# Kernel optimization log

Hardware: AMD Instinct MI355X
Metric: run time of the kernel (lower is better)

## Reference

```python
import jax, jax.numpy as jnp
import numpy as np

N = 100000   # nodes
E = 600000   # edges
D = 128      # in_dim == out_dim
ED = 6       # edge_dim
LN_EPS = 1e-5


def setup_inputs() -> dict:
    key = jax.random.key(0)
    ks = jax.random.split(key, 12)
    s = 1.0 / np.sqrt(D)
    se = 1.0 / np.sqrt(ED)
    return {
        "x": jax.random.normal(ks[0], (N, D), dtype=jnp.float32),
        "edge_index": jax.random.randint(ks[1], (2, E), 0, N, dtype=jnp.int64),
        "edge_attr": jax.random.normal(ks[2], (E, ED), dtype=jnp.float32),
        "batch": jnp.zeros((N,), dtype=jnp.int64),
        "W_e": jax.random.uniform(ks[3], (ED, D), jnp.float32, -se, se),
        "b_e": jax.random.uniform(ks[4], (D,), jnp.float32, -se, se),
        "eps": jnp.zeros((), dtype=jnp.float32),  # GINE train_eps init 0
        "W1": jax.random.uniform(ks[5], (D, D), jnp.float32, -s, s),
        "b1": jax.random.uniform(ks[6], (D,), jnp.float32, -s, s),
        "W2": jax.random.uniform(ks[7], (D, D), jnp.float32, -s, s),
        "b2": jax.random.uniform(ks[8], (D,), jnp.float32, -s, s),
        "gamma": jnp.ones((D,), dtype=jnp.float32),
        "beta": jnp.zeros((D,), dtype=jnp.float32),
    }


def reference(x, edge_index, edge_attr, batch, W_e, b_e, eps, W1, b1, W2, b2, gamma, beta):
    src, dst = edge_index[0], edge_index[1]
    # edge embedding: Linear(edge_dim -> in_dim)
    edge_emb = edge_attr @ W_e + b_e                      # [E, D]
    # GINEConv message: ReLU(x_j + edge_emb), scatter-add to target nodes
    msg = jax.nn.relu(x[src] + edge_emb)                  # [E, D]
    agg = jax.ops.segment_sum(msg, dst, num_segments=N)   # [N, D]
    h = (1.0 + eps) * x + agg                             # [N, D]
    # GINE nn: Linear -> ReLU -> Linear
    h = jax.nn.relu(h @ W1 + b1) @ W2 + b2                # [N, D]
    # LayerNorm over feature dim
    mu = jnp.mean(h, axis=-1, keepdims=True)
    var = jnp.var(h, axis=-1, keepdims=True)
    h = (h - mu) * jax.lax.rsqrt(var + LN_EPS) * gamma + beta
    # activation=True -> ReLU; dropout identity in eval mode
    return jax.nn.relu(h)
```

## Files before the change

### kernel.cpp

```cpp
#include <hip/hip_runtime.h>
#include <stdint.h>

#define NN 100000
#define EE 600000
#define DD 128

typedef _Float16 half8 __attribute__((ext_vector_type(8)));
typedef _Float16 h2 __attribute__((ext_vector_type(2)));
typedef float f32x4 __attribute__((ext_vector_type(4)));

static __device__ __forceinline__ uint32_t pack2(float a, float b) {
    h2 h; h.x = (_Float16)a; h.y = (_Float16)b;
    return __builtin_bit_cast(uint32_t, h);
}
static __device__ __forceinline__ h2 cvt22(float2 f) {
    h2 r; r.x = (_Float16)f.x; r.y = (_Float16)f.y; return r;
}
static __device__ __forceinline__ h2 bc_lo(h2 v) { h2 r; r.x = v.x; r.y = v.x; return r; }
static __device__ __forceinline__ h2 bc_hi(h2 v) { h2 r; r.x = v.y; r.y = v.y; return r; }

static __device__ __forceinline__ uint32_t edge_msg2(uint32_t rY, uint32_t rZ, uint32_t rW,
                                                     uint32_t xv, uint32_t bb,
                                                     uint32_t w0, uint32_t w1, uint32_t w2,
                                                     uint32_t w3, uint32_t w4, uint32_t w5)
{
    uint32_t m;
    asm("v_pk_fma_f16 %0, %1, %2, %3 op_sel:[0,0,0] op_sel_hi:[0,1,1]"
        : "=v"(m) : "v"(rY), "v"(w0), "v"(bb));
    asm("v_pk_fma_f16 %0, %1, %2, %0 op_sel:[1,0,0] op_sel_hi:[1,1,1]" : "+v"(m) : "v"(rY), "v"(w1));
    asm("v_pk_fma_f16 %0, %1, %2, %0 op_sel:[0,0,0] op_sel_hi:[0,1,1]" : "+v"(m) : "v"(rZ), "v"(w2));
    asm("v_pk_fma_f16 %0, %1, %2, %0 op_sel:[1,0,0] op_sel_hi:[1,1,1]" : "+v"(m) : "v"(rZ), "v"(w3));
    asm("v_pk_fma_f16 %0, %1, %2, %0 op_sel:[0,0,0] op_sel_hi:[0,1,1]" : "+v"(m) : "v"(rW), "v"(w4));
    asm("v_pk_fma_f16 %0, %1, %2, %0 op_sel:[1,0,0] op_sel_hi:[1,1,1]" : "+v"(m) : "v"(rW), "v"(w5));
    asm("v_pk_add_f16 %0, %0, %1" : "+v"(m) : "v"(xv));
    asm("v_pk_max_f16 %0, %0, 0" : "+v"(m));
    return m;
}

#define NB_HIST ((EE + 255) / 256)
#define NB_CONV (NN * DD / 4 / 256)
template<bool CONV>
__global__ __launch_bounds__(256)
void setup_kernel(const int* __restrict__ ei, const float* __restrict__ x,
                  const float* __restrict__ W1, const float* __restrict__ W2,
                  int* __restrict__ counts, uint32_t* __restrict__ xh,
                  _Float16* __restrict__ w1h, _Float16* __restrict__ w2h)
{
    const int nbc = CONV ? NB_CONV : 0;
    const int b = blockIdx.x, tid = threadIdx.x;
    if (b < NB_HIST) {
        int e = b * 256 + tid;
        if (e < EE) atomicAdd(&counts[ei[EE + e]], 1);
    } else if (CONV && b < NB_HIST + nbc) {
        int i = (b - NB_HIST) * 256 + tid;
        float4 v = ((const float4*)x)[i];
        uint2 o; o.x = pack2(v.x, v.y); o.y = pack2(v.z, v.w);
        ((uint2*)xh)[i] = o;
    } else {
        int t = (b - NB_HIST - nbc) * 256 + tid;
        if (t < 2 * DD * DD) {
            int which = t >> 14;
            int idx = t & (DD * DD - 1);
            int k = idx >> 7, d = idx & 127;
            float wv = (which ? W2 : W1)[k * DD + d];
            int kt = k >> 5, kr = k & 31;
            int grp = kr >> 3, j = kr & 7;
            int nt = d >> 4, cc = d & 15;
            int off = ((kt * 8 + nt) * 64 + grp * 16 + cc) * 8 + j;
            (which ? w2h : w1h)[off] = (_Float16)wv;
        }
    }
}

__global__ __launch_bounds__(256)
void scan_blocks(const int* __restrict__ counts, int* __restrict__ startv,
                 int* __restrict__ bsum)
{
    const int t = threadIdx.x;
    const int idx = blockIdx.x * 1024 + t * 4;
    int4 v = {0, 0, 0, 0};
    if (idx < NN) v = *(const int4*)(counts + idx);
    int s1 = v.x + v.y, s2 = s1 + v.z, s3 = s2 + v.w;
    const int lane = t & 63;
    int q = s3;
#pragma unroll
    for (int off = 1; off < 64; off <<= 1) {
        int u = __shfl_up(q, off, 64);
        if (lane >= off) q += u;
    }
    __shared__ int wsum[4];
    if (lane == 63) wsum[t >> 6] = q;
    __syncthreads();
    const int w = t >> 6;
    int pre = 0;
    if (w > 0) pre += wsum[0];
    if (w > 1) pre += wsum[1];
    if (w > 2) pre += wsum[2];
    const int excl = (q - s3) + pre;
    if (idx < NN) {
        int4 o = {excl, excl + v.x, excl + s1, excl + s2};
        *(int4*)(startv + idx) = o;
    }
    __syncthreads();
    if (t == 0) bsum[blockIdx.x] = wsum[0] + wsum[1] + wsum[2] + wsum[3];
}

__global__ __launch_bounds__(128)
void scan_top(const int* __restrict__ bsum, int* __restrict__ boff)
{
    __shared__ int sm[128];
    const int t = threadIdx.x;
    const int NB = (NN + 1023) / 1024;
    int v = (t < NB) ? bsum[t] : 0;
    sm[t] = v;
    __syncthreads();
#pragma unroll
    for (int off = 1; off < 128; off <<= 1) {
        int u = (t >= off) ? sm[t - off] : 0;
        __syncthreads();
        sm[t] += u;
        __syncthreads();
    }
    boff[t] = sm[t] - v;
}

__global__ __launch_bounds__(256)
void scatter_rec(const int* __restrict__ ei, const float* __restrict__ ea,
                 const int* __restrict__ start, const int* __restrict__ boff,
                 int* __restrict__ cursor, float* __restrict__ rec)
{
    int e = blockIdx.x * 256 + threadIdx.x;
    if (e >= EE) return;
    int dst = ei[EE + e];
    int src = ei[e];
    int pos = start[dst] + boff[dst >> 10] + atomicAdd(&cursor[dst], 1);
    const float2* eap = (const float2*)(ea + e * 6);
    float2 e01 = eap[0];
    float2 e23 = eap[1];
    float2 e45 = eap[2];
    float4 r;
    r.x = __int_as_float(src << 6);
    r.y = __uint_as_float(pack2(e01.x, e01.y));
    r.z = __uint_as_float(pack2(e23.x, e23.y));
    r.w = __uint_as_float(pack2(e45.x, e45.y));
    *(float4*)(rec + (size_t)pos * 4) = r;
}

#define NWAVE 8192
__global__ __launch_bounds__(256)
void agg_stream(const uint32_t* __restrict__ xh,
                const float4* __restrict__ rec, const float* __restrict__ We,
                const float* __restrict__ be, const int* __restrict__ start,
                const int* __restrict__ boff, const float* __restrict__ epsp,
                uint32_t* __restrict__ h0h)
{
    const int w = blockIdx.x * 4 + (threadIdx.x >> 6);
    const int lane = threadIdx.x & 63;
    const int d0 = lane * 2;
    const uint32_t w0u = __builtin_bit_cast(uint32_t, cvt22(*(const float2*)(We + 0 * DD + d0)));
    const uint32_t w1u = __builtin_bit_cast(uint32_t, cvt22(*(const float2*)(We + 1 * DD + d0)));
    const uint32_t w2u = __builtin_bit_cast(uint32_t, cvt22(*(const float2*)(We + 2 * DD + d0)));
    const uint32_t w3u = __builtin_bit_cast(uint32_t, cvt22(*(const float2*)(We + 3 * DD + d0)));
    const uint32_t w4u = __builtin_bit_cast(uint32_t, cvt22(*(const float2*)(We + 4 * DD + d0)));
    const uint32_t w5u = __builtin_bit_cast(uint32_t, cvt22(*(const float2*)(We + 5 * DD + d0)));
    const uint32_t bbu = __builtin_bit_cast(uint32_t, cvt22(*(const float2*)(be + d0)));
    const float sc = 1.0f + epsp[0];
    const int n0 = (int)(((long long)w * NN) >> 13);
    const int n1 = (int)(((long long)(w + 1) * NN) >> 13);
    const int span = n1 - n0;

    int gs = 0;
    {
        int nidx = n0 + lane;
        if (lane <= span) {
            gs = (nidx < NN) ? (start[nidx] + boff[nidx >> 10]) : EE;
        }
    }
    const int ebase = __shfl(gs, 0, 64);
    const int eend  = __shfl(gs, span, 64);

    int n = n0;
    int nstop = __shfl(gs, 1, 64);
    h2 xnh = __builtin_bit_cast(h2, xh[((uint32_t)n0 << 6) + lane]);
    float ax = 0.f, ay = 0.f;

#define STEP(K, MK)                                                              \
    {                                                                            \
        const int ek = e + K;                                                    \
        if (ek < eend) {                                                         \
            while (ek >= nstop) {                                                \
                h0h[(size_t)n * 64 + lane] =                                     \
                    pack2(fmaf(sc, (float)xnh.x, ax), fmaf(sc, (float)xnh.y, ay)); \
                ax = 0.f; ay = 0.f; ++n;                                         \
                xnh = __builtin_bit_cast(h2, xh[((uint32_t)n << 6) + lane]);     \
                nstop = __shfl(gs, n - n0 + 1, 64);                              \
            }                                                                    \
            h2 mh = __builtin_bit_cast(h2, MK);                                  \
            ax += (float)mh.x; ay += (float)mh.y;                                \
        }                                                                        \
    }

    for (int e = ebase; e < eend; e += 8) {
        const int last = eend - 1;
        int idx[8];
        float4 r[8];
        uint32_t xv[8], m[8];
#pragma unroll
        for (int k = 0; k < 8; ++k) {
            int ik = e + k;
            idx[k] = ik < eend ? ik : last;
        }
#pragma unroll
        for (int k = 0; k < 8; ++k) r[k] = rec[idx[k]];
#pragma unroll
        for (int k = 0; k < 8; ++k)
            xv[k] = xh[(uint32_t)__float_as_int(r[k].x) + lane];
#pragma unroll
        for (int k = 0; k < 8; ++k)
            m[k] = edge_msg2(__float_as_uint(r[k].y), __float_as_uint(r[k].z),
                             __float_as_uint(r[k].w), xv[k], bbu,
                             w0u, w1u, w2u, w3u, w4u, w5u);
        STEP(0, m[0])
        STEP(1, m[1])
        STEP(2, m[2])
        STEP(3, m[3])
        STEP(4, m[4])
        STEP(5, m[5])
        STEP(6, m[6])
        STEP(7, m[7])
    }
#undef STEP

    while (n < n1) {
        h0h[(size_t)n * 64 + lane] = pack2(fmaf(sc, (float)xnh.x, ax), fmaf(sc, (float)xnh.y, ay));
        ax = 0.f; ay = 0.f; ++n;
        if (n < n1) xnh = __builtin_bit_cast(h2, xh[((uint32_t)n << 6) + lane]);
    }
}

__global__ __launch_bounds__(256)
void agg_pk(const float* __restrict__ x, const float* __restrict__ rec,
            const float* __restrict__ We, const float* __restrict__ be,
            const int* __restrict__ start, const int* __restrict__ boff,
            const int* __restrict__ counts, const float* __restrict__ epsp,
            uint32_t* __restrict__ h0h)
{
    const int w = blockIdx.x * 4 + (threadIdx.x >> 6);
    const int lane = threadIdx.x & 63;
    const int d0 = lane * 2;
    const h2 w0h = cvt22(*(const float2*)(We + 0 * DD + d0));
    const h2 w1h = cvt22(*(const float2*)(We + 1 * DD + d0));
    const h2 w2h = cvt22(*(const float2*)(We + 2 * DD + d0));
    const h2 w3h = cvt22(*(const float2*)(We + 3 * DD + d0));
    const h2 w4h = cvt22(*(const float2*)(We + 4 * DD + d0));
    const h2 w5h = cvt22(*(const float2*)(We + 5 * DD + d0));
    const h2 bbh = cvt22(*(const float2*)(be + d0));
    h2 zero2; zero2.x = (_Float16)0.f; zero2.y = (_Float16)0.f;
    const float sc = 1.0f + epsp[0];
    const int n0 = (int)(((long long)w * NN) >> 13);
    const int n1 = (int)(((long long)(w + 1) * NN) >> 13);

    for (int n = n0; n < n1; ++n) {
        const int begin = start[n] + boff[n >> 10];
        const int cnt = counts[n];
        const float4* rp = (const float4*)rec + begin;
        float ax = 0.f, ay = 0.f;
        for (int i = 0; i < cnt; ++i) {
            float4 r = rp[i];
            int s64 = __float_as_int(r.x);
            h2 c01 = __builtin_bit_cast(h2, r.y);
            h2 c23 = __builtin_bit_cast(h2, r.z);
            h2 c45 = __builtin_bit_cast(h2, r.w);
            h2 emb = bbh;
            emb = bc_lo(c01) * w0h + emb;
            emb = bc_hi(c01) * w1h + emb;
            emb = bc_lo(c23) * w2h + emb;
            emb = bc_hi(c23) * w3h + emb;
            emb = bc_lo(c45) * w4h + emb;
            emb = bc_hi(c45) * w5h + emb;
            h2 m = emb + cvt22(*(const float2*)(x + (size_t)s64 * 2 + d0));
            m = __builtin_elementwise_max(m, zero2);
            ax += (float)m.x;
            ay += (float)m.y;
        }
        float2 xn = *(const float2*)(x + (size_t)n * DD + d0);
        h0h[(size_t)n * 64 + lane] = pack2(fmaf(sc, xn.x, ax), fmaf(sc, xn.y, ay));
    }
}

__global__ __launch_bounds__(256)
void prep_w(const float* __restrict__ W1, const float* __restrict__ W2,
            _Float16* __restrict__ w1h, _Float16* __restrict__ w2h)
{
    int t = blockIdx.x * 256 + threadIdx.x;
    if (t >= 2 * DD * DD) return;
    int which = t >> 14;
    int idx = t & (DD * DD - 1);
    int k = idx >> 7, d = idx & 127;
    float wv = (which ? W2 : W1)[k * DD + d];
    int kt = k >> 5, kr = k & 31;
    int grp = kr >> 3, j = kr & 7;
    int nt = d >> 4, cc = d & 15;
    int off = ((kt * 8 + nt) * 64 + grp * 16 + cc) * 8 + j;
    (which ? w2h : w1h)[off] = (_Float16)wv;
}

__global__ __launch_bounds__(256)
void edge_kernel(const float* __restrict__ x, const int* __restrict__ ei,
                 const float* __restrict__ ea, const float* __restrict__ We,
                 const float* __restrict__ be, float* agg)
{
    int tid = blockIdx.x * 256 + threadIdx.x;
    int d0 = (tid & 31) * 4;
    float4 w0 = *(const float4*)(We + 0 * DD + d0);
    float4 w1 = *(const float4*)(We + 1 * DD + d0);
    float4 w2 = *(const float4*)(We + 2 * DD + d0);
    float4 w3 = *(const float4*)(We + 3 * DD + d0);
    float4 w4 = *(const float4*)(We + 4 * DD + d0);
    float4 w5 = *(const float4*)(We + 5 * DD + d0);
    float4 bb = *(const float4*)(be + d0);
    int estride = (gridDim.x * 256) >> 5;
    for (int e = tid >> 5; e < EE; e += estride) {
        int src = ei[e];
        int dst = ei[EE + e];
        const float2* eap = (const float2*)(ea + e * 6);
        float2 e01 = eap[0];
        float2 e23 = eap[1];
        float2 e45 = eap[2];
        float4 xj = *(const float4*)(x + (size_t)src * DD + d0);
        float mx = xj.x + bb.x + e01.x*w0.x + e01.y*w1.x + e23.x*w2.x + e23.y*w3.x + e45.x*w4.x + e45.y*w5.x;
        float my = xj.y + bb.y + e01.x*w0.y + e01.y*w1.y + e23.x*w2.y + e23.y*w3.y + e45.x*w4.y + e45.y*w5.y;
        float mz = xj.z + bb.z + e01.x*w0.z + e01.y*w1.z + e23.x*w2.z + e23.y*w3.z + e45.x*w4.z + e45.y*w5.z;
        float mw = xj.w + bb.w + e01.x*w0.w + e01.y*w1.w + e23.x*w2.w + e23.y*w3.w + e45.x*w4.w + e45.y*w5.w;
        float* ap = agg + (size_t)dst * DD + d0;
        atomicAdd(ap + 0, fmaxf(mx, 0.f));
        atomicAdd(ap + 1, fmaxf(my, 0.f));
        atomicAdd(ap + 2, fmaxf(mz, 0.f));
        atomicAdd(ap + 3, fmaxf(mw, 0.f));
    }
}

__global__ __launch_bounds__(256)
void node_f16(const uint32_t* __restrict__ h0h,
              const _Float16* __restrict__ w1h, const _Float16* __restrict__ w2h,
              const float* __restrict__ b1, const float* __restrict__ b2,
              const float* __restrict__ gamma, const float* __restrict__ beta,
              float* __restrict__ out)
{
    __shared__ _Float16 h1buf[4][16 * 128];
    const int wv = threadIdx.x >> 6;
    const int l  = threadIdx.x & 63;
    const int lm = l & 15;
    const int lg = l >> 4;
    const int rbase = blockIdx.x * 128 + wv * 32;

    float gam[8], bet[8];
#pragma unroll
    for (int nt = 0; nt < 8; ++nt) {
        gam[nt] = gamma[nt * 16 + lm];
        bet[nt] = beta[nt * 16 + lm];
    }

    for (int t = 0; t < 2; ++t) {
        const int r0 = rbase + t * 16;
        int arow = r0 + lm;
        if (arow >= NN) arow = NN - 1;

        half8 a1[4];
#pragma unroll
        for (int kt = 0; kt < 4; ++kt) {
            const int kb = kt * 32 + lg * 8;
            a1[kt] = *(const half8*)((const _Float16*)h0h + (size_t)arow * DD + kb);
        }

        f32x4 acc[8];
#pragma unroll
        for (int nt = 0; nt < 8; ++nt) { acc[nt][0]=0.f; acc[nt][1]=0.f; acc[nt][2]=0.f; acc[nt][3]=0.f; }
#pragma unroll
        for (int kt = 0; kt < 4; ++kt) {
#pragma unroll
            for (int nt = 0; nt < 8; ++nt) {
                half8 bh = *(const half8*)(w1h + ((size_t)((kt * 8 + nt) * 64 + l)) * 8);
                acc[nt] = __builtin_amdgcn_mfma_f32_16x16x32_f16(a1[kt], bh, acc[nt], 0, 0, 0);
            }
        }

        _Float16* hb = h1buf[wv];
#pragma unroll
        for (int nt = 0; nt < 8; ++nt) {
            const int col = nt * 16 + lm;
            const float bias = b1[col];
#pragma unroll
            for (int q = 0; q < 4; ++q) {
                const int row = lg * 4 + q;
                float v1 = fmaxf(acc[nt][q] + bias, 0.f);
                hb[row * 128 + (col ^ ((row & 7) << 4))] = (_Float16)v1;
            }
        }

        half8 a2[4];
        {
            const int sw = (lm & 7) << 4;
            const _Float16* rowp = hb + lm * 128;
#pragma unroll
            for (int kt = 0; kt < 4; ++kt) {
                const int kb = kt * 32 + lg * 8;
                a2[kt] = *(const half8*)(rowp + (kb ^ sw));
            }
        }

        f32x4 acc2[8];
#pragma unroll
        for (int nt = 0; nt < 8; ++nt) { acc2[nt][0]=0.f; acc2[nt][1]=0.f; acc2[nt][2]=0.f; acc2[nt][3]=0.f; }
#pragma unroll
        for (int kt = 0; kt < 4; ++kt) {
#pragma unroll
            for (int nt = 0; nt < 8; ++nt) {
                half8 bh = *(const half8*)(w2h + ((size_t)((kt * 8 + nt) * 64 + l)) * 8);
                acc2[nt] = __builtin_amdgcn_mfma_f32_16x16x32_f16(a2[kt], bh, acc2[nt], 0, 0, 0);
            }
        }

        float vv[8][4];
        float sums[4] = {0,0,0,0}, sqs[4] = {0,0,0,0};
#pragma unroll
        for (int nt = 0; nt < 8; ++nt) {
            const int col = nt * 16 + lm;
            const float bias = b2[col];
#pragma unroll
            for (int q = 0; q < 4; ++q) {
                float v2 = acc2[nt][q] + bias;
                vv[nt][q] = v2;
                sums[q] += v2;
                sqs[q]  += v2 * v2;
            }
        }
#pragma unroll
        for (int m = 1; m < 16; m <<= 1) {
#pragma unroll
            for (int q = 0; q < 4; ++q) {
                sums[q] += __shfl_xor(sums[q], m, 64);
                sqs[q]  += __shfl_xor(sqs[q],  m, 64);
            }
        }
#pragma unroll
        for (int q = 0; q < 4; ++q) {
            const int grow = r0 + lg * 4 + q;
            if (grow < NN) {
                const float mu  = sums[q] * (1.f / 128.f);
                const float var = sqs[q] * (1.f / 128.f) - mu * mu;
                const float rs  = rsqrtf(var + 1e-5f);
#pragma unroll
                for (int nt = 0; nt < 8; ++nt) {
                    out[(size_t)grow * DD + nt * 16 + lm] =
                        fmaxf((vv[nt][q] - mu) * rs * gam[nt] + bet[nt], 0.f);
                }
            }
        }
    }
}

__global__ __launch_bounds__(256)
void node2c(const float* __restrict__ aggp, const float* __restrict__ xp,
            const _Float16* __restrict__ w1h, const _Float16* __restrict__ w2h,
            const float* __restrict__ b1, const float* __restrict__ b2,
            const float* __restrict__ gamma, const float* __restrict__ beta,
            const float* __restrict__ epsp, float* __restrict__ out)
{
    __shared__ _Float16 h1buf[4][16 * 128];
    const int wv = threadIdx.x >> 6;
    const int l  = threadIdx.x & 63;
    const int lm = l & 15;
    const int lg = l >> 4;
    const int rbase = blockIdx.x * 128 + wv * 32;

    float gam[8], bet[8];
#pragma unroll
    for (int nt = 0; nt < 8; ++nt) {
        gam[nt] = gamma[nt * 16 + lm];
        bet[nt] = beta[nt * 16 + lm];
    }

    for (int t = 0; t < 2; ++t) {
        const int r0 = rbase + t * 16;
        int arow = r0 + lm;
        if (arow >= NN) arow = NN - 1;

        half8 a1[4];
#pragma unroll
        for (int kt = 0; kt < 4; ++kt) {
            const int kb = kt * 32 + lg * 8;
            const float4* hp = (const float4*)(aggp + (size_t)arow * DD + kb);
            float4 p0 = hp[0], p1 = hp[1];
            const float scale = 1.0f + epsp[0];
            const float4* xr = (const float4*)(xp + (size_t)arow * DD + kb);
            float4 x0 = xr[0], x1 = xr[1];
            float v[8] = { x0.x*scale+p0.x, x0.y*scale+p0.y, x0.z*scale+p0.z, x0.w*scale+p0.w,
                           x1.x*scale+p1.x, x1.y*scale+p1.y, x1.z*scale+p1.z, x1.w*scale+p1.w };
#pragma unroll
            for (int j = 0; j < 8; ++j) a1[kt][j] = (_Float16)v[j];
        }

        f32x4 acc[8];
#pragma unroll
        for (int nt = 0; nt < 8; ++nt) { acc[nt][0]=0.f; acc[nt][1]=0.f; acc[nt][2]=0.f; acc[nt][3]=0.f; }
#pragma unroll
        for (int kt = 0; kt < 4; ++kt) {
#pragma unroll
            for (int nt = 0; nt < 8; ++nt) {
                half8 bh = *(const half8*)(w1h + ((size_t)((kt * 8 + nt) * 64 + l)) * 8);
                acc[nt] = __builtin_amdgcn_mfma_f32_16x16x32_f16(a1[kt], bh, acc[nt], 0, 0, 0);
            }
        }

        _Float16* hb = h1buf[wv];
#pragma unroll
        for (int nt = 0; nt < 8; ++nt) {
            const int col = nt * 16 + lm;
            const float bias = b1[col];
#pragma unroll
            for (int q = 0; q < 4; ++q) {
                const int row = lg * 4 + q;
                float v1 = fmaxf(acc[nt][q] + bias, 0.f);
                hb[row * 128 + (col ^ ((row & 7) << 4))] = (_Float16)v1;
            }
        }

        half8 a2[4];
        {
            const int sw = (lm & 7) << 4;
            const _Float16* rowp = hb + lm * 128;
#pragma unroll
            for (int kt = 0; kt < 4; ++kt) {
                const int kb = kt * 32 + lg * 8;
                a2[kt] = *(const half8*)(rowp + (kb ^ sw));
            }
        }

        f32x4 acc2[8];
#pragma unroll
        for (int nt = 0; nt < 8; ++nt) { acc2[nt][0]=0.f; acc2[nt][1]=0.f; acc2[nt][2]=0.f; acc2[nt][3]=0.f; }
#pragma unroll
        for (int kt = 0; kt < 4; ++kt) {
#pragma unroll
            for (int nt = 0; nt < 8; ++nt) {
                half8 bh = *(const half8*)(w2h + ((size_t)((kt * 8 + nt) * 64 + l)) * 8);
                acc2[nt] = __builtin_amdgcn_mfma_f32_16x16x32_f16(a2[kt], bh, acc2[nt], 0, 0, 0);
            }
        }

        float vv[8][4];
        float sums[4] = {0,0,0,0}, sqs[4] = {0,0,0,0};
#pragma unroll
        for (int nt = 0; nt < 8; ++nt) {
            const int col = nt * 16 + lm;
            const float bias = b2[col];
#pragma unroll
            for (int q = 0; q < 4; ++q) {
                float v2 = acc2[nt][q] + bias;
                vv[nt][q] = v2;
                sums[q] += v2;
                sqs[q]  += v2 * v2;
            }
        }
#pragma unroll
        for (int m = 1; m < 16; m <<= 1) {
#pragma unroll
            for (int q = 0; q < 4; ++q) {
                sums[q] += __shfl_xor(sums[q], m, 64);
                sqs[q]  += __shfl_xor(sqs[q],  m, 64);
            }
        }
#pragma unroll
        for (int q = 0; q < 4; ++q) {
            const int grow = r0 + lg * 4 + q;
            if (grow < NN) {
                const float mu  = sums[q] * (1.f / 128.f);
                const float var = sqs[q] * (1.f / 128.f) - mu * mu;
                const float rs  = rsqrtf(var + 1e-5f);
#pragma unroll
                for (int nt = 0; nt < 8; ++nt) {
                    out[(size_t)grow * DD + nt * 16 + lm] =
                        fmaxf((vv[nt][q] - mu) * rs * gam[nt] + bet[nt], 0.f);
                }
            }
        }
    }
}

extern "C" void kernel_launch(void* const* d_in, const int* in_sizes, int n_in,
                              void* d_out, int out_size, void* d_ws, size_t ws_size,
                              hipStream_t stream) {
    (void)in_sizes; (void)n_in; (void)out_size;
    const float* x     = (const float*)d_in[0];
    const int*   ei    = (const int*)d_in[1];
    const float* ea    = (const float*)d_in[2];
    const float* We    = (const float*)d_in[4];
    const float* be    = (const float*)d_in[5];
    const float* epsp  = (const float*)d_in[6];
    const float* W1    = (const float*)d_in[7];
    const float* b1    = (const float*)d_in[8];
    const float* W2    = (const float*)d_in[9];
    const float* b2    = (const float*)d_in[10];
    const float* gamma = (const float*)d_in[11];
    const float* beta  = (const float*)d_in[12];
    float* out = (float*)d_out;

    char* ws = (char*)d_ws;
    _Float16* w1h = (_Float16*)ws;
    _Float16* w2h = w1h + DD * DD;
    size_t off = 2 * (size_t)DD * DD * sizeof(_Float16);
    int* counts = (int*)(ws + off);   off += (size_t)NN * 4;
    int* cursor = (int*)(ws + off);   off += (size_t)NN * 4;
    int* start  = (int*)(ws + off);   off += (size_t)NN * 4;
    int* bsum   = (int*)(ws + off);   off += 512;
    int* boff   = (int*)(ws + off);   off += 512;
    float* rec  = (float*)(ws + off); off += (size_t)EE * 16;
    uint32_t* h0h = (uint32_t*)(ws + off); off += (size_t)NN * DD * 2;
    const size_t need_h0 = off;
    uint32_t* xh  = (uint32_t*)(ws + off); off += (size_t)NN * DD * 2;
    const size_t need_xh = off;

    const int node_blocks = (NN + 127) / 128;
    const int NBLK = (NN + 1023) / 1024;

    if (ws_size >= need_h0) {
        const bool conv = (ws_size >= need_xh);
        hipMemsetAsync(counts, 0, 2 * (size_t)NN * 4, stream);
        if (conv) {
            setup_kernel<true><<<NB_HIST + NB_CONV + 128, 256, 0, stream>>>(
                ei, x, W1, W2, counts, xh, w1h, w2h);
        } else {
            setup_kernel<false><<<NB_HIST + 128, 256, 0, stream>>>(
                ei, x, W1, W2, counts, xh, w1h, w2h);
        }
        scan_blocks<<<NBLK, 256, 0, stream>>>(counts, start, bsum);
        scan_top<<<1, 128, 0, stream>>>(bsum, boff);
        scatter_rec<<<(EE + 255) / 256, 256, 0, stream>>>(ei, ea, start, boff, cursor, rec);
        if (conv) {
            agg_stream<<<NWAVE / 4, 256, 0, stream>>>(xh, (const float4*)rec, We, be,
                                                      start, boff, epsp, h0h);
        } else {
            agg_pk<<<NWAVE / 4, 256, 0, stream>>>(x, rec, We, be, start, boff,
                                                  counts, epsp, h0h);
        }
        node_f16<<<node_blocks, 256, 0, stream>>>(h0h, w1h, w2h, b1, b2, gamma, beta, out);
    } else {
        hipMemsetAsync(d_out, 0, (size_t)NN * DD * sizeof(float), stream);
        prep_w<<<(2 * DD * DD + 255) / 256, 256, 0, stream>>>(W1, W2, w1h, w2h);
        edge_kernel<<<2048, 256, 0, stream>>>(x, ei, ea, We, be, out);
        node2c<<<node_blocks, 256, 0, stream>>>(out, x, w1h, w2h, b1, b2,
                                                gamma, beta, epsp, out);
    }
}
```

Measured before the change: 160.5 us.

## Fuse CSR aggregation with node MLP and LayerNorm in one kernel

Replaces the separate aggregation kernel (which wrote an fp16 h0 buffer to global memory) and the node MLP kernel with one fused kernel. Each wave aggregates 16 nodes into a swizzled LDS tile, then runs both MFMA GEMMs and the LayerNorm directly from LDS. It also drops the fp16 pre-conversion of x and instead gathers fp32 x rows, converting them in registers. This removes the h0 round trip, one launch and the x conversion pass. In exchange the gathers read twice as many bytes, and load balance across waves is now by fixed node count rather than by wave.

```diff
diff --git a/kernel.cpp b/kernel.cpp
--- a/kernel.cpp
+++ b/kernel.cpp
@@ -38,26 +38,18 @@
 }
 
 #define NB_HIST ((EE + 255) / 256)
-#define NB_CONV (NN * DD / 4 / 256)
-template<bool CONV>
 __global__ __launch_bounds__(256)
-void setup_kernel(const int* __restrict__ ei, const float* __restrict__ x,
-                  const float* __restrict__ W1, const float* __restrict__ W2,
-                  int* __restrict__ counts, uint32_t* __restrict__ xh,
-                  _Float16* __restrict__ w1h, _Float16* __restrict__ w2h)
-{
-    const int nbc = CONV ? NB_CONV : 0;
+void setup2(const int* __restrict__ ei,
+            const float* __restrict__ W1, const float* __restrict__ W2,
+            int* __restrict__ counts,
+            _Float16* __restrict__ w1h, _Float16* __restrict__ w2h)
+{
     const int b = blockIdx.x, tid = threadIdx.x;
     if (b < NB_HIST) {
         int e = b * 256 + tid;
         if (e < EE) atomicAdd(&counts[ei[EE + e]], 1);
-    } else if (CONV && b < NB_HIST + nbc) {
-        int i = (b - NB_HIST) * 256 + tid;
-        float4 v = ((const float4*)x)[i];
-        uint2 o; o.x = pack2(v.x, v.y); o.y = pack2(v.z, v.w);
-        ((uint2*)xh)[i] = o;
     } else {
-        int t = (b - NB_HIST - nbc) * 256 + tid;
+        int t = (b - NB_HIST) * 256 + tid;
         if (t < 2 * DD * DD) {
             int which = t >> 14;
             int idx = t & (DD * DD - 1);
@@ -146,145 +138,215 @@
     *(float4*)(rec + (size_t)pos * 4) = r;
 }
 
-#define NWAVE 8192
-__global__ __launch_bounds__(256)
-void agg_stream(const uint32_t* __restrict__ xh,
-                const float4* __restrict__ rec, const float* __restrict__ We,
-                const float* __restrict__ be, const int* __restrict__ start,
-                const int* __restrict__ boff, const float* __restrict__ epsp,
-                uint32_t* __restrict__ h0h)
-{
-    const int w = blockIdx.x * 4 + (threadIdx.x >> 6);
+__global__ __launch_bounds__(256, 4)
+void fused_an(const float* __restrict__ x, const float4* __restrict__ rec,
+              const float* __restrict__ We, const float* __restrict__ be,
+              const int* __restrict__ start, const int* __restrict__ boff,
+              const float* __restrict__ epsp,
+              const _Float16* __restrict__ w1h, const _Float16* __restrict__ w2h,
+              const float* __restrict__ b1, const float* __restrict__ b2,
+              const float* __restrict__ gamma, const float* __restrict__ beta,
+              float* __restrict__ out)
+{
+    __shared__ _Float16 hbuf[4][16 * 128];
+    const int wv = threadIdx.x >> 6;
     const int lane = threadIdx.x & 63;
-    const int d0 = lane * 2;
-    const uint32_t w0u = __builtin_bit_cast(uint32_t, cvt22(*(const float2*)(We + 0 * DD + d0)));
-    const uint32_t w1u = __builtin_bit_cast(uint32_t, cvt22(*(const float2*)(We + 1 * DD + d0)));
-    const uint32_t w2u = __builtin_bit_cast(uint32_t, cvt22(*(const float2*)(We + 2 * DD + d0)));
-    const uint32_t w3u = __builtin_bit_cast(uint32_t, cvt22(*(const float2*)(We + 3 * DD + d0)));
-    const uint32_t w4u = __builtin_bit_cast(uint32_t, cvt22(*(const float2*)(We + 4 * DD + d0)));
-    const uint32_t w5u = __builtin_bit_cast(uint32_t, cvt22(*(const float2*)(We + 5 * DD + d0)));
-    const uint32_t bbu = __builtin_bit_cast(uint32_t, cvt22(*(const float2*)(be + d0)));
-    const float sc = 1.0f + epsp[0];
-    const int n0 = (int)(((long long)w * NN) >> 13);
-    const int n1 = (int)(((long long)(w + 1) * NN) >> 13);
-    const int span = n1 - n0;
-
-    int gs = 0;
+    const int n0w = blockIdx.x * 64 + wv * 16;
+    _Float16* hb = hbuf[wv];
+
+    if (n0w < NN) {
+        int n1w = n0w + 16; if (n1w > NN) n1w = NN;
+        const int span = n1w - n0w;
+        const int d0 = lane * 2;
+        const uint32_t w0u = __builtin_bit_cast(uint32_t, cvt22(*(const float2*)(We + 0 * DD + d0)));
+        const uint32_t w1u = __builtin_bit_cast(uint32_t, cvt22(*(const float2*)(We + 1 * DD + d0)));
+        const uint32_t w2u = __builtin_bit_cast(uint32_t, cvt22(*(const float2*)(We + 2 * DD + d0)));
+        const uint32_t w3u = __builtin_bit_cast(uint32_t, cvt22(*(const float2*)(We + 3 * DD + d0)));
+        const uint32_t w4u = __builtin_bit_cast(uint32_t, cvt22(*(const float2*)(We + 4 * DD + d0)));
+        const uint32_t w5u = __builtin_bit_cast(uint32_t, cvt22(*(const float2*)(We + 5 * DD + d0)));
+        const uint32_t bbu = __builtin_bit_cast(uint32_t, cvt22(*(const float2*)(be + d0)));
+        const float sc = 1.0f + epsp[0];
+
+        int gs = 0;
+        {
+            int nidx = n0w + lane;
+            if (lane <= span) gs = (nidx < NN) ? (start[nidx] + boff[nidx >> 10]) : EE;
+        }
+        const int ebase = __shfl(gs, 0, 64);
+        const int eend  = __shfl(gs, span, 64);
+
+        int n = n0w;
+        int nstop = __shfl(gs, 1, 64);
+        float2 xn = *(const float2*)(x + (size_t)n0w * DD + d0);
+        float ax = 0.f, ay = 0.f;
+
+#define FLUSH_H0()                                                               \
+        {                                                                        \
+            const int row = n - n0w;                                             \
+            *(uint32_t*)&hb[row * 128 + (d0 ^ ((row & 7) << 4))] =               \
+                pack2(fmaf(sc, xn.x, ax), fmaf(sc, xn.y, ay));                   \
+        }
+
+#define STEP(K, MK)                                                              \
+        {                                                                        \
+            const int ek = e + K;                                                \
+            if (ek < eend) {                                                     \
+                while (ek >= nstop) {                                            \
+                    FLUSH_H0();                                                  \
+                    ax = 0.f; ay = 0.f; ++n;                                     \
+                    xn = *(const float2*)(x + (size_t)n * DD + d0);              \
+                    nstop = __shfl(gs, n - n0w + 1, 64);                         \
+                }                                                                \
+                h2 mh = __builtin_bit_cast(h2, MK);                              \
+                ax += (float)mh.x; ay += (float)mh.y;                            \
+            }                                                                    \
+        }
+
+        for (int e = ebase; e < eend; e += 8) {
+            const int last = eend - 1;
+            int idx[8];
+            float4 r[8];
+            uint32_t xv[8], m[8];
+#pragma unroll
+            for (int k = 0; k < 8; ++k) {
+                int ik = e + k;
+                idx[k] = ik < eend ? ik : last;
+            }
+#pragma unroll
+            for (int k = 0; k < 8; ++k) r[k] = rec[idx[k]];
+#pragma unroll
+            for (int k = 0; k < 8; ++k) {
+                float2 xf = *(const float2*)(x + ((size_t)(uint32_t)__float_as_int(r[k].x)) * 2 + d0);
+                xv[k] = __builtin_bit_cast(uint32_t, cvt22(xf));
+            }
+#pragma unroll
+            for (int k = 0; k < 8; ++k)
+                m[k] = edge_msg2(__float_as_uint(r[k].y), __float_as_uint(r[k].z),
+                                 __float_as_uint(r[k].w), xv[k], bbu,
+                                 w0u, w1u, w2u, w3u, w4u, w5u);
+            STEP(0, m[0])
+            STEP(1, m[1])
+            STEP(2, m[2])
+            STEP(3, m[3])
+            STEP(4, m[4])
+            STEP(5, m[5])
+            STEP(6, m[6])
+            STEP(7, m[7])
+        }
+#undef STEP
+
+        while (n < n1w) {
+            FLUSH_H0();
+            ax = 0.f; ay = 0.f; ++n;
+            if (n < n1w) xn = *(const float2*)(x + (size_t)n * DD + d0);
+        }
+#undef FLUSH_H0
+    }
+
+    const int l  = lane;
+    const int lm = l & 15;
+    const int lg = l >> 4;
+    const int r0 = n0w;
+
+    half8 a1[4];
     {
-        int nidx = n0 + lane;
-        if (lane <= span) {
-            gs = (nidx < NN) ? (start[nidx] + boff[nidx >> 10]) : EE;
-        }
-    }
-    const int ebase = __shfl(gs, 0, 64);
-    const int eend  = __shfl(gs, span, 64);
-
-    int n = n0;
-    int nstop = __shfl(gs, 1, 64);
-    h2 xnh = __builtin_bit_cast(h2, xh[((uint32_t)n0 << 6) + lane]);
-    float ax = 0.f, ay = 0.f;
-
-#define STEP(K, MK)                                                              \
-    {                                                                            \
-        const int ek = e + K;                                                    \
-        if (ek < eend) {                                                         \
-            while (ek >= nstop) {                                                \
-                h0h[(size_t)n * 64 + lane] =                                     \
-                    pack2(fmaf(sc, (float)xnh.x, ax), fmaf(sc, (float)xnh.y, ay)); \
-                ax = 0.f; ay = 0.f; ++n;                                         \
-                xnh = __builtin_bit_cast(h2, xh[((uint32_t)n << 6) + lane]);     \
-                nstop = __shfl(gs, n - n0 + 1, 64);                              \
-            }                                                                    \
-            h2 mh = __builtin_bit_cast(h2, MK);                                  \
-            ax += (float)mh.x; ay += (float)mh.y;                                \
-        }                                                                        \
-    }
-
-    for (int e = ebase; e < eend; e += 8) {
-        const int last = eend - 1;
-        int idx[8];
-        float4 r[8];
-        uint32_t xv[8], m[8];
-#pragma unroll
-        for (int k = 0; k < 8; ++k) {
-            int ik = e + k;
-            idx[k] = ik < eend ? ik : last;
-        }
-#pragma unroll
-        for (int k = 0; k < 8; ++k) r[k] = rec[idx[k]];
-#pragma unroll
-        for (int k = 0; k < 8; ++k)
-            xv[k] = xh[(uint32_t)__float_as_int(r[k].x) + lane];
-#pragma unroll
-        for (int k = 0; k < 8; ++k)
-            m[k] = edge_msg2(__float_as_uint(r[k].y), __float_as_uint(r[k].z),
-                             __float_as_uint(r[k].w), xv[k], bbu,
-                             w0u, w1u, w2u, w3u, w4u, w5u);
-        STEP(0, m[0])
-        STEP(1, m[1])
-        STEP(2, m[2])
-        STEP(3, m[3])
-        STEP(4, m[4])
-        STEP(5, m[5])
-        STEP(6, m[6])
-        STEP(7, m[7])
-    }
-#undef STEP
-
-    while (n < n1) {
-        h0h[(size_t)n * 64 + lane] = pack2(fmaf(sc, (float)xnh.x, ax), fmaf(sc, (float)xnh.y, ay));
-        ax = 0.f; ay = 0.f; ++n;
-        if (n < n1) xnh = __builtin_bit_cast(h2, xh[((uint32_t)n << 6) + lane]);
-    }
-}
-
-__global__ __launch_bounds__(256)
-void agg_pk(const float* __restrict__ x, const float* __restrict__ rec,
-            const float* __restrict__ We, const float* __restrict__ be,
-            const int* __restrict__ start, const int* __restrict__ boff,
-            const int* __restrict__ counts, const float* __restrict__ epsp,
-            uint32_t* __restrict__ h0h)
-{
-    const int w = blockIdx.x * 4 + (threadIdx.x >> 6);
-    const int lane = threadIdx.x & 63;
-    const int d0 = lane * 2;
-    const h2 w0h = cvt22(*(const float2*)(We + 0 * DD + d0));
-    const h2 w1h = cvt22(*(const float2*)(We + 1 * DD + d0));
-    const h2 w2h = cvt22(*(const float2*)(We + 2 * DD + d0));
-    const h2 w3h = cvt22(*(const float2*)(We + 3 * DD + d0));
-    const h2 w4h = cvt22(*(const float2*)(We + 4 * DD + d0));
-    const h2 w5h = cvt22(*(const float2*)(We + 5 * DD + d0));
-    const h2 bbh = cvt22(*(const float2*)(be + d0));
-    h2 zero2; zero2.x = (_Float16)0.f; zero2.y = (_Float16)0.f;
-    const float sc = 1.0f + epsp[0];
-    const int n0 = (int)(((long long)w * NN) >> 13);
-    const int n1 = (int)(((long long)(w + 1) * NN) >> 13);
-
-    for (int n = n0; n < n1; ++n) {
-        const int begin = start[n] + boff[n >> 10];
-        const int cnt = counts[n];
-        const float4* rp = (const float4*)rec + begin;
-        float ax = 0.f, ay = 0.f;
-        for (int i = 0; i < cnt; ++i) {
-            float4 r = rp[i];
-            int s64 = __float_as_int(r.x);
-            h2 c01 = __builtin_bit_cast(h2, r.y);
-            h2 c23 = __builtin_bit_cast(h2, r.z);
-            h2 c45 = __builtin_bit_cast(h2, r.w);
-            h2 emb = bbh;
-            emb = bc_lo(c01) * w0h + emb;
-            emb = bc_hi(c01) * w1h + emb;
-            emb = bc_lo(c23) * w2h + emb;
-            emb = bc_hi(c23) * w3h + emb;
-            emb = bc_lo(c45) * w4h + emb;
-            emb = bc_hi(c45) * w5h + emb;
-            h2 m = emb + cvt22(*(const float2*)(x + (size_t)s64 * 2 + d0));
-            m = __builtin_elementwise_max(m, zero2);
-            ax += (float)m.x;
-            ay += (float)m.y;
-        }
-        float2 xn = *(const float2*)(x + (size_t)n * DD + d0);
-        h0h[(size_t)n * 64 + lane] = pack2(fmaf(sc, xn.x, ax), fmaf(sc, xn.y, ay));
+        const int sw = (lm & 7) << 4;
+        const _Float16* rowp = hb + lm * 128;
+#pragma unroll
+        for (int kt = 0; kt < 4; ++kt) {
+            const int kb = kt * 32 + lg * 8;
+            a1[kt] = *(const half8*)(rowp + (kb ^ sw));
+        }
+    }
+
+    f32x4 acc[8];
+#pragma unroll
+    for (int nt = 0; nt < 8; ++nt) { acc[nt][0]=0.f; acc[nt][1]=0.f; acc[nt][2]=0.f; acc[nt][3]=0.f; }
+#pragma unroll
+    for (int kt = 0; kt < 4; ++kt) {
+#pragma unroll
+        for (int nt = 0; nt < 8; ++nt) {
+            half8 bh = *(const half8*)(w1h + ((size_t)((kt * 8 + nt) * 64 + l)) * 8);
+            acc[nt] = __builtin_amdgcn_mfma_f32_16x16x32_f16(a1[kt], bh, acc[nt], 0, 0, 0);
+        }
+    }
+
+#pragma unroll
+    for (int nt = 0; nt < 8; ++nt) {
+        const int col = nt * 16 + lm;
+        const float bias = b1[col];
+#pragma unroll
+        for (int q = 0; q < 4; ++q) {
+            const int row = lg * 4 + q;
+            float v1 = fmaxf(acc[nt][q] + bias, 0.f);
+            hb[row * 128 + (col ^ ((row & 7) << 4))] = (_Float16)v1;
+        }
+    }
+
+    half8 a2[4];
+    {
+        const int sw = (lm & 7) << 4;
+        const _Float16* rowp = hb + lm * 128;
+#pragma unroll
+        for (int kt = 0; kt < 4; ++kt) {
+            const int kb = kt * 32 + lg * 8;
+            a2[kt] = *(const half8*)(rowp + (kb ^ sw));
+        }
+    }
+
+    f32x4 acc2[8];
+#pragma unroll
+    for (int nt = 0; nt < 8; ++nt) { acc2[nt][0]=0.f; acc2[nt][1]=0.f; acc2[nt][2]=0.f; acc2[nt][3]=0.f; }
+#pragma unroll
+    for (int kt = 0; kt < 4; ++kt) {
+#pragma unroll
+        for (int nt = 0; nt < 8; ++nt) {
+            half8 bh = *(const half8*)(w2h + ((size_t)((kt * 8 + nt) * 64 + l)) * 8);
+            acc2[nt] = __builtin_amdgcn_mfma_f32_16x16x32_f16(a2[kt], bh, acc2[nt], 0, 0, 0);
+        }
+    }
+
+    float sums[4] = {0,0,0,0}, sqs[4] = {0,0,0,0};
+#pragma unroll
+    for (int nt = 0; nt < 8; ++nt) {
+        const float bias = b2[nt * 16 + lm];
+#pragma unroll
+        for (int q = 0; q < 4; ++q) {
+            float v2 = acc2[nt][q] + bias;
+            sums[q] += v2;
+            sqs[q]  += v2 * v2;
+        }
+    }
+#pragma unroll
+    for (int m = 1; m < 16; m <<= 1) {
+#pragma unroll
+        for (int q = 0; q < 4; ++q) {
+            sums[q] += __shfl_xor(sums[q], m, 64);
+            sqs[q]  += __shfl_xor(sqs[q],  m, 64);
+        }
+    }
+
+    float gam[8], bet[8], b2r[8];
+#pragma unroll
+    for (int nt = 0; nt < 8; ++nt) {
+        gam[nt] = gamma[nt * 16 + lm];
+        bet[nt] = beta[nt * 16 + lm];
+        b2r[nt] = b2[nt * 16 + lm];
+    }
+#pragma unroll
+    for (int q = 0; q < 4; ++q) {
+        const int grow = r0 + lg * 4 + q;
+        if (grow < NN) {
+            const float mu  = sums[q] * (1.f / 128.f);
+            const float var = sqs[q] * (1.f / 128.f) - mu * mu;
+            const float rs  = rsqrtf(var + 1e-5f);
+#pragma unroll
+            for (int nt = 0; nt < 8; ++nt) {
+                float v2 = acc2[nt][q] + b2r[nt];
+                out[(size_t)grow * DD + nt * 16 + lm] =
+                    fmaxf((v2 - mu) * rs * gam[nt] + bet[nt], 0.f);
+            }
+        }
     }
 }
 
@@ -341,126 +403,6 @@
 }
 
 __global__ __launch_bounds__(256)
-void node_f16(const uint32_t* __restrict__ h0h,
-              const _Float16* __restrict__ w1h, const _Float16* __restrict__ w2h,
-              const float* __restrict__ b1, const float* __restrict__ b2,
-              const float* __restrict__ gamma, const float* __restrict__ beta,
-              float* __restrict__ out)
-{
-    __shared__ _Float16 h1buf[4][16 * 128];
-    const int wv = threadIdx.x >> 6;
-    const int l  = threadIdx.x & 63;
-    const int lm = l & 15;
-    const int lg = l >> 4;
-    const int rbase = blockIdx.x * 128 + wv * 32;
-
-    float gam[8], bet[8];
-#pragma unroll
-    for (int nt = 0; nt < 8; ++nt) {
-        gam[nt] = gamma[nt * 16 + lm];
-        bet[nt] = beta[nt * 16 + lm];
-    }
-
-    for (int t = 0; t < 2; ++t) {
-        const int r0 = rbase + t * 16;
-        int arow = r0 + lm;
-        if (arow >= NN) arow = NN - 1;
-
-        half8 a1[4];
-#pragma unroll
-        for (int kt = 0; kt < 4; ++kt) {
-            const int kb = kt * 32 + lg * 8;
-            a1[kt] = *(const half8*)((const _Float16*)h0h + (size_t)arow * DD + kb);
-        }
-
-        f32x4 acc[8];
-#pragma unroll
-        for (int nt = 0; nt < 8; ++nt) { acc[nt][0]=0.f; acc[nt][1]=0.f; acc[nt][2]=0.f; acc[nt][3]=0.f; }
-#pragma unroll
-        for (int kt = 0; kt < 4; ++kt) {
-#pragma unroll
-            for (int nt = 0; nt < 8; ++nt) {
-                half8 bh = *(const half8*)(w1h + ((size_t)((kt * 8 + nt) * 64 + l)) * 8);
-                acc[nt] = __builtin_amdgcn_mfma_f32_16x16x32_f16(a1[kt], bh, acc[nt], 0, 0, 0);
-            }
-        }
-
-        _Float16* hb = h1buf[wv];
-#pragma unroll
-        for (int nt = 0; nt < 8; ++nt) {
-            const int col = nt * 16 + lm;
-            const float bias = b1[col];
-#pragma unroll
-            for (int q = 0; q < 4; ++q) {
-                const int row = lg * 4 + q;
-                float v1 = fmaxf(acc[nt][q] + bias, 0.f);
-                hb[row * 128 + (col ^ ((row & 7) << 4))] = (_Float16)v1;
-            }
-        }
-
-        half8 a2[4];
-        {
-            const int sw = (lm & 7) << 4;
-            const _Float16* rowp = hb + lm * 128;
-#pragma unroll
-            for (int kt = 0; kt < 4; ++kt) {
-                const int kb = kt * 32 + lg * 8;
-                a2[kt] = *(const half8*)(rowp + (kb ^ sw));
-            }
-        }
-
-        f32x4 acc2[8];
-#pragma unroll
-        for (int nt = 0; nt < 8; ++nt) { acc2[nt][0]=0.f; acc2[nt][1]=0.f; acc2[nt][2]=0.f; acc2[nt][3]=0.f; }
-#pragma unroll
-        for (int kt = 0; kt < 4; ++kt) {
-#pragma unroll
-            for (int nt = 0; nt < 8; ++nt) {
-                half8 bh = *(const half8*)(w2h + ((size_t)((kt * 8 + nt) * 64 + l)) * 8);
-                acc2[nt] = __builtin_amdgcn_mfma_f32_16x16x32_f16(a2[kt], bh, acc2[nt], 0, 0, 0);
-            }
-        }
-
-        float vv[8][4];
-        float sums[4] = {0,0,0,0}, sqs[4] = {0,0,0,0};
-#pragma unroll
-        for (int nt = 0; nt < 8; ++nt) {
-            const int col = nt * 16 + lm;
-            const float bias = b2[col];
-#pragma unroll
-            for (int q = 0; q < 4; ++q) {
-                float v2 = acc2[nt][q] + bias;
-                vv[nt][q] = v2;
-                sums[q] += v2;
-                sqs[q]  += v2 * v2;
-            }
-        }
-#pragma unroll
-        for (int m = 1; m < 16; m <<= 1) {
-#pragma unroll
-            for (int q = 0; q < 4; ++q) {
-                sums[q] += __shfl_xor(sums[q], m, 64);
-                sqs[q]  += __shfl_xor(sqs[q],  m, 64);
-            }
-        }
-#pragma unroll
-        for (int q = 0; q < 4; ++q) {
-            const int grow = r0 + lg * 4 + q;
-            if (grow < NN) {
-                const float mu  = sums[q] * (1.f / 128.f);
-                const float var = sqs[q] * (1.f / 128.f) - mu * mu;
-                const float rs  = rsqrtf(var + 1e-5f);
-#pragma unroll
-                for (int nt = 0; nt < 8; ++nt) {
-                    out[(size_t)grow * DD + nt * 16 + lm] =
-                        fmaxf((vv[nt][q] - mu) * rs * gam[nt] + bet[nt], 0.f);
-                }
-            }
-        }
-    }
-}
-
-__global__ __launch_bounds__(256)
 void node2c(const float* __restrict__ aggp, const float* __restrict__ xp,
             const _Float16* __restrict__ w1h, const _Float16* __restrict__ w2h,
             const float* __restrict__ b1, const float* __restrict__ b2,
@@ -616,35 +558,21 @@
     int* bsum   = (int*)(ws + off);   off += 512;
     int* boff   = (int*)(ws + off);   off += 512;
     float* rec  = (float*)(ws + off); off += (size_t)EE * 16;
-    uint32_t* h0h = (uint32_t*)(ws + off); off += (size_t)NN * DD * 2;
-    const size_t need_h0 = off;
-    uint32_t* xh  = (uint32_t*)(ws + off); off += (size_t)NN * DD * 2;
-    const size_t need_xh = off;
+    const size_t need_rec = off;
 
     const int node_blocks = (NN + 127) / 128;
+    const int fused_blocks = (NN + 63) / 64;
     const int NBLK = (NN + 1023) / 1024;
 
-    if (ws_size >= need_h0) {
-        const bool conv = (ws_size >= need_xh);
+    if (ws_size >= need_rec) {
         hipMemsetAsync(counts, 0, 2 * (size_t)NN * 4, stream);
-        if (conv) {
-            setup_kernel<true><<<NB_HIST + NB_CONV + 128, 256, 0, stream>>>(
-                ei, x, W1, W2, counts, xh, w1h, w2h);
-        } else {
-            setup_kernel<false><<<NB_HIST + 128, 256, 0, stream>>>(
-                ei, x, W1, W2, counts, xh, w1h, w2h);
-        }
+        setup2<<<NB_HIST + 128, 256, 0, stream>>>(ei, W1, W2, counts, w1h, w2h);
         scan_blocks<<<NBLK, 256, 0, stream>>>(counts, start, bsum);
         scan_top<<<1, 128, 0, stream>>>(bsum, boff);
         scatter_rec<<<(EE + 255) / 256, 256, 0, stream>>>(ei, ea, start, boff, cursor, rec);
-        if (conv) {
-            agg_stream<<<NWAVE / 4, 256, 0, stream>>>(xh, (const float4*)rec, We, be,
-                                                      start, boff, epsp, h0h);
-        } else {
-            agg_pk<<<NWAVE / 4, 256, 0, stream>>>(x, rec, We, be, start, boff,
-                                                  counts, epsp, h0h);
-        }
-        node_f16<<<node_blocks, 256, 0, stream>>>(h0h, w1h, w2h, b1, b2, gamma, beta, out);
+        fused_an<<<fused_blocks, 256, 0, stream>>>(x, (const float4*)rec, We, be,
+                                                   start, boff, epsp, w1h, w2h,
+                                                   b1, b2, gamma, beta, out);
     } else {
         hipMemsetAsync(d_out, 0, (size_t)NN * DD * sizeof(float), stream);
         prep_w<<<(2 * DD * DD + 255) / 256, 256, 0, stream>>>(W1, W2, w1h, w2h);
```

Result: faster. 150.8 us (-6.0%).
